# Performance work log

Measured on AMD Instinct MI355X. Metric: run time of the kernel, lower is better.

The kernel has to match this reference:

```python
import jax, jax.numpy as jnp
import numpy as np

N_HEAD = 8
D_MODEL = 128  # per-head dim == d_model in this 'interpretable' MHA
B, S = 2, 2048
LN_EPS = 1e-3  # keras LayerNormalization default epsilon


def setup_inputs() -> dict:
    key = jax.random.key(0)
    ks = jax.random.split(key, 8)
    sc = 1.0 / np.sqrt(D_MODEL)
    q = jax.random.normal(ks[0], (B, S, D_MODEL), jnp.float32)
    k = jax.random.normal(ks[1], (B, S, D_MODEL), jnp.float32)
    v = jax.random.normal(ks[2], (B, S, D_MODEL), jnp.float32)
    # multiplicative causal mask (lower-triangular ones), broadcast over B,H
    mask = jnp.tril(jnp.ones((S, S), jnp.float32))[None, None, :, :]
    Wq = jax.random.normal(ks[3], (D_MODEL, N_HEAD * D_MODEL), jnp.float32) * sc
    Wk = jax.random.normal(ks[4], (D_MODEL, N_HEAD * D_MODEL), jnp.float32) * sc
    Wv = jax.random.normal(ks[5], (D_MODEL, N_HEAD * D_MODEL), jnp.float32) * sc
    Wo = jax.random.normal(ks[6], (N_HEAD * D_MODEL, D_MODEL), jnp.float32) * sc
    gamma = jnp.ones((D_MODEL,), jnp.float32)
    beta = jnp.zeros((D_MODEL,), jnp.float32)
    return {"q": q, "k": k, "v": v, "mask": mask, "Wq": Wq, "Wk": Wk,
            "Wv": Wv, "Wo": Wo, "gamma": gamma, "beta": beta}


def reference(q, k, v, mask, Wq, Wk, Wv, Wo, gamma, beta):
    b = q.shape[0]
    # projections -> [B, H, S, D]
    def split_heads(x):
        return x.reshape(b, -1, N_HEAD, D_MODEL).transpose(0, 2, 1, 3)
    qs = split_heads(q @ Wq)
    ks_ = split_heads(k @ Wk)
    vs = split_heads(v @ Wv)
    scores = jnp.einsum('bhqd,bhkd->bhqk', qs, ks_) / jnp.sqrt(jnp.float32(D_MODEL))
    scores = scores * mask  # multiplicative mask (NOT additive -inf)
    attn = jax.nn.softmax(scores, axis=-1)
    # dropout layers are identity at inference
    out = jnp.einsum('bhqk,bhkd->bhqd', attn, vs)
    out = out.transpose(0, 2, 1, 3).reshape(b, -1, N_HEAD * D_MODEL)
    out = out @ Wo
    # keras LayerNorm (axis=-1, eps=1e-3)
    mu = jnp.mean(out, axis=-1, keepdims=True)
    var = jnp.var(out, axis=-1, keepdims=True)
    out = (out - mu) * jax.lax.rsqrt(var + LN_EPS) * gamma + beta
    return out
```

## Files before the change

### kernel.cpp

```cpp
#include <hip/hip_runtime.h>
#include <math.h>

#define B 2
#define S 2048
#define H 8
#define D 128
#define DM 1024
#define BH 16

typedef unsigned short u16;
typedef __attribute__((ext_vector_type(8))) short bf16x8;
typedef __attribute__((ext_vector_type(8))) unsigned short u16x8;
typedef __attribute__((ext_vector_type(4))) float f32x4;

__device__ __forceinline__ float bf2f(u16 x) {
    union { unsigned u; float f; } c; c.u = ((unsigned)x) << 16; return c.f;
}
__device__ __forceinline__ u16 f2bf(float f) {
    union { unsigned u; float f; } c; c.f = f;
    unsigned u = c.u; u += 0x7fffu + ((u >> 16) & 1u);
    return (u16)(u >> 16);
}
__device__ __forceinline__ u16 ftr(float f) {
    union { unsigned u; float f; } c; c.f = f;
    return (u16)(c.u >> 16);
}

#define MFMA16(a, b, c) __builtin_amdgcn_mfma_f32_16x16x32_bf16((a), (b), (c), 0, 0, 0)

__global__ __launch_bounds__(256) void prep_kernel(
    const float* __restrict__ Wq, const float* __restrict__ Wk, const float* __restrict__ Wv,
    const float* __restrict__ Wo, u16* __restrict__ WT, u16* __restrict__ WoT)
{
    __shared__ __align__(16) u16 Wl[128][132];
    int tid = threadIdx.x, by = blockIdx.x;
    if (by < 16) {
        int k0 = by * 64;
#pragma unroll
        for (int i = 0; i < 8; i++) {
            int e = i * 256 + tid; int kk = e >> 5, n4 = e & 31;
            float4 w4 = *(const float4*)&Wo[(size_t)(k0 + kk) * D + n4 * 4];
            ushort4 p; p.x = ftr(w4.x); p.y = ftr(w4.y); p.z = ftr(w4.z); p.w = ftr(w4.w);
            *(ushort4*)&Wl[kk][n4 * 4] = p;
        }
        __syncthreads();
#pragma unroll
        for (int i = 0; i < 4; i++) {
            int e = i * 256 + tid; int n = e >> 3, ko = e & 7;
            u16x8 g;
#pragma unroll
            for (int j = 0; j < 8; j++) g[j] = Wl[ko * 8 + j][n];
            *(u16x8*)&WoT[(size_t)n * DM + k0 + ko * 8] = g;
        }
    } else {
        int tile = by - 16;
        int t = tile >> 3, h = tile & 7;
        const float* W = (t == 0) ? Wq : (t == 1) ? Wk : Wv;
        int col0 = h * 128;
#pragma unroll
        for (int i = 0; i < 16; i++) {
            int e = i * 256 + tid; int kk = e >> 5, n4 = e & 31;
            float4 w4 = *(const float4*)&W[(size_t)kk * DM + col0 + n4 * 4];
            ushort4 p; p.x = ftr(w4.x); p.y = ftr(w4.y); p.z = ftr(w4.z); p.w = ftr(w4.w);
            *(ushort4*)&Wl[kk][n4 * 4] = p;
        }
        __syncthreads();
        u16* WTt = WT + (size_t)tile * (128 * 128);
#pragma unroll
        for (int i = 0; i < 8; i++) {
            int e = i * 256 + tid; int n = e >> 4, ko = e & 15;
            u16x8 g;
#pragma unroll
            for (int j = 0; j < 8; j++) g[j] = Wl[ko * 8 + j][n];
            *(u16x8*)&WTt[(size_t)n * 128 + ko * 8] = g;
        }
    }
}

__global__ __launch_bounds__(256) void proj_kernel(
    const float* __restrict__ q, const float* __restrict__ k, const float* __restrict__ v,
    const u16* __restrict__ WT,
    u16* __restrict__ Qo, u16* __restrict__ Ko, u16* __restrict__ VTo,
    float* __restrict__ Csum)
{
    __shared__ __align__(16) u16 Xs[64][136];
    __shared__ __align__(16) u16 Ws[128][136];
    int tid = threadIdx.x;
    int m0 = blockIdx.x * 64;
    int by = blockIdx.y;
    int t = by >> 3;
    int h = by & 7;
    const float* X = (t == 0) ? q : (t == 1) ? k : v;
    const u16* WTt = WT + (size_t)(t * 8 + h) * (128 * 128);

#pragma unroll
    for (int i = 0; i < 8; i++) {
        int e = i * 256 + tid; int r = e >> 5, c4 = e & 31;
        float4 x4 = *(const float4*)&X[(size_t)(m0 + r) * D + c4 * 4];
        ushort4 p; p.x = ftr(x4.x); p.y = ftr(x4.y); p.z = ftr(x4.z); p.w = ftr(x4.w);
        *(ushort4*)&Xs[r][c4 * 4] = p;
    }
#pragma unroll
    for (int i = 0; i < 8; i++) {
        int e = i * 256 + tid; int n = e >> 4, c8 = e & 15;
        *(u16x8*)&Ws[n][c8 * 8] = *(const u16x8*)&WTt[(size_t)n * 128 + c8 * 8];
    }
    __syncthreads();

    int w = tid >> 6, lane = tid & 63, quad = lane >> 4, ln = lane & 15;
    bf16x8 aX[4];
#pragma unroll
    for (int ks = 0; ks < 4; ks++)
        aX[ks] = *(const bf16x8*)&Xs[w * 16 + ln][ks * 32 + quad * 8];

    f32x4 zero = {0.f, 0.f, 0.f, 0.f};
    f32x4 acc[8];
#pragma unroll
    for (int nt = 0; nt < 8; nt++) acc[nt] = zero;

#pragma unroll
    for (int ks = 0; ks < 4; ks++) {
        bf16x8 bW[8];
#pragma unroll
        for (int nt = 0; nt < 8; nt++)
            bW[nt] = *(const bf16x8*)&Ws[nt * 16 + ln][ks * 32 + quad * 8];
#pragma unroll
        for (int nt = 0; nt < 8; nt++)
            acc[nt] = MFMA16(aX[ks], bW[nt], acc[nt]);
    }

    int bb = m0 >> 11, ss0 = m0 & 2047;
    int bh = bb * 8 + h;
    __syncthreads();
    if (t < 2) {
        u16 (*Ct)[136] = Xs;
        u16* O = (t == 0) ? Qo : Ko;
#pragma unroll
        for (int nt = 0; nt < 8; nt++)
#pragma unroll
            for (int r = 0; r < 4; r++)
                Ct[w * 16 + quad * 4 + r][nt * 16 + ln] = f2bf(acc[nt][r]);
        __syncthreads();
#pragma unroll
        for (int i = 0; i < 4; i++) {
            int e = i * 256 + tid; int r = e >> 4, c8 = e & 15;
            *(u16x8*)&O[((size_t)bh * S + ss0 + r) * D + c8 * 8] = *(const u16x8*)&Ct[r][c8 * 8];
        }
    } else {
        u16 (*Ct)[68] = (u16 (*)[68])&Xs[0][0];
#pragma unroll
        for (int nt = 0; nt < 8; nt++)
#pragma unroll
            for (int r = 0; r < 4; r++)
                Ct[nt * 16 + ln][w * 16 + quad * 4 + r] = f2bf(acc[nt][r]);
        __syncthreads();
#pragma unroll
        for (int i = 0; i < 4; i++) {
            int e = i * 256 + tid; int dloc = e >> 3, c8 = e & 7;
            *(u16x8*)&VTo[((size_t)bh * D + dloc) * S + ss0 + c8 * 8] =
                *(const u16x8*)&Ct[dloc][c8 * 8];
        }
        if (tid < 128) {
            int d = tid;
            float s = 0.f;
#pragma unroll
            for (int i = 0; i < 8; i++) {
                u16x8 v8 = *(const u16x8*)&Ct[d][i * 8];
#pragma unroll
                for (int j = 0; j < 8; j++) s += bf2f(v8[j]);
            }
            Csum[((size_t)bh * 32 + (ss0 >> 6)) * D + d] = s;
        }
    }
}

__global__ __launch_bounds__(512, 2) void attn_kernel(
    const u16* __restrict__ Qb, const u16* __restrict__ Kb, const u16* __restrict__ VTg,
    const float* __restrict__ Csum, u16* __restrict__ HOb)
{
    __shared__ __align__(16) u16 Qs[2][64][136];
    __shared__ __align__(16) u16 Ks[128][136];
    __shared__ __align__(16) u16 Vt[128][136];
    __shared__ __align__(16) u16 Ps[2][64][136];
    __shared__ float Lred[2][4][64];

    int tid = threadIdx.x;
    int bh = blockIdx.x;
    int bx = blockIdx.y;
    int nhi = (31 - bx) / 2 + 1, nlo = bx / 2 + 1;
    int w = tid >> 6, qt = w >> 2, wq = w & 3, lane = tid & 63, quad = lane >> 4, ln = lane & 15;
    int qb = qt ? bx : (31 - bx);
    int q0 = qb * 64;
    int nq = qt ? nlo : nhi;
    const u16* Qp  = Qb  + (size_t)bh * S * D;
    const u16* Kp  = Kb  + (size_t)bh * S * D;
    const u16* VTp = VTg + (size_t)bh * D * S;

#pragma unroll
    for (int i = 0; i < 4; i++) {
        int e = i * 512 + tid; int r2 = e >> 4, c8 = e & 15;
        int qtt = r2 >> 6, r = r2 & 63;
        int q0s = (qtt ? bx : (31 - bx)) * 64;
        *(u16x8*)&Qs[qtt][r][c8 * 8] = *(const u16x8*)&Qp[(size_t)(q0s + r) * D + c8 * 8];
    }
    __syncthreads();
    bf16x8 aQ[4][4];
#pragma unroll
    for (int rf = 0; rf < 4; rf++)
#pragma unroll
        for (int ks = 0; ks < 4; ks++)
            aQ[rf][ks] = *(const bf16x8*)&Qs[qt][rf * 16 + ln][ks * 32 + quad * 8];

    f32x4 zero = {0.f, 0.f, 0.f, 0.f};
    f32x4 accPV[4][2], acc_l[4];
#pragma unroll
    for (int rf = 0; rf < 4; rf++) { accPV[rf][0] = zero; accPV[rf][1] = zero; acc_l[rf] = zero; }
    bf16x8 bOnes;
#pragma unroll
    for (int j = 0; j < 8; j++) bOnes[j] = (short)0x3F80;
    const float scale = 0.08838834764831845f;

    for (int kt = 0; kt < nhi; kt++) {
        __syncthreads();
        int k0 = kt * 128;
#pragma unroll
        for (int i = 0; i < 4; i++) {
            int e = i * 512 + tid; int r = e >> 4, c8 = e & 15;
            *(u16x8*)&Ks[r][c8 * 8] = *(const u16x8*)&Kp[(size_t)(k0 + r) * D + c8 * 8];
        }
#pragma unroll
        for (int i = 0; i < 4; i++) {
            int e = i * 512 + tid; int dd = e >> 4, c8 = e & 15;
            *(u16x8*)&Vt[dd][c8 * 8] = *(const u16x8*)&VTp[(size_t)dd * S + k0 + c8 * 8];
        }
        __syncthreads();
        bool active = (qt == 0) || (kt < nlo);
        if (active) {
            f32x4 s[4][2];
#pragma unroll
            for (int rf = 0; rf < 4; rf++) { s[rf][0] = zero; s[rf][1] = zero; }
#pragma unroll
            for (int ks = 0; ks < 4; ks++) {
                bf16x8 b0 = *(const bf16x8*)&Ks[wq * 32 + ln][ks * 32 + quad * 8];
                bf16x8 b1 = *(const bf16x8*)&Ks[wq * 32 + 16 + ln][ks * 32 + quad * 8];
#pragma unroll
                for (int rf = 0; rf < 4; rf++) {
                    s[rf][0] = MFMA16(aQ[rf][ks], b0, s[rf][0]);
                    s[rf][1] = MFMA16(aQ[rf][ks], b1, s[rf][1]);
                }
            }
#pragma unroll
            for (int rf = 0; rf < 4; rf++)
#pragma unroll
                for (int ct = 0; ct < 2; ct++) {
                    int col = k0 + wq * 32 + ct * 16 + ln;
                    int rowb = q0 + rf * 16 + quad * 4;
#pragma unroll
                    for (int r = 0; r < 4; r++) {
                        float tv = (col <= rowb + r) ? s[rf][ct][r] : 0.f;
                        float p = __expf(tv * scale);
                        Ps[qt][rf * 16 + quad * 4 + r][wq * 32 + ct * 16 + ln] = f2bf(p);
                    }
                }
        }
        __syncthreads();
        if (active) {
#pragma unroll
            for (int ks = 0; ks < 4; ks++) {
                bf16x8 aP[4];
#pragma unroll
                for (int rf = 0; rf < 4; rf++)
                    aP[rf] = *(const bf16x8*)&Ps[qt][rf * 16 + ln][ks * 32 + quad * 8];
                bf16x8 v0 = *(const bf16x8*)&Vt[wq * 32 + ln][ks * 32 + quad * 8];
                bf16x8 v1 = *(const bf16x8*)&Vt[wq * 32 + 16 + ln][ks * 32 + quad * 8];
                if (ks == wq) {
#pragma unroll
                    for (int rf = 0; rf < 4; rf++) acc_l[rf] = MFMA16(aP[rf], bOnes, acc_l[rf]);
                }
#pragma unroll
                for (int rf = 0; rf < 4; rf++) {
                    accPV[rf][0] = MFMA16(aP[rf], v0, accPV[rf][0]);
                    accPV[rf][1] = MFMA16(aP[rf], v1, accPV[rf][1]);
                }
            }
        }
    }

    __syncthreads();
    if (ln == 0) {
#pragma unroll
        for (int rf = 0; rf < 4; rf++)
#pragma unroll
            for (int r = 0; r < 4; r++)
                Lred[qt][wq][rf * 16 + quad * 4 + r] = acc_l[rf][r];
    }
    __syncthreads();

    int nt64 = 2 * nq;
    float suf0 = 0.f, suf1 = 0.f;
    for (int c = 31; c >= nt64; c--) {
        const float* cp = &Csum[((size_t)(bh * 32 + c)) * D + wq * 32];
        suf0 += cp[ln];
        suf1 += cp[16 + ln];
    }
    int scount = S - nq * 128;
    int b = bh >> 3, h = bh & 7;
#pragma unroll
    for (int rf = 0; rf < 4; rf++)
#pragma unroll
        for (int r = 0; r < 4; r++) {
            int row = rf * 16 + quad * 4 + r;
            int srow = q0 + row;
            float l = Lred[qt][0][row] + Lred[qt][1][row] + Lred[qt][2][row] + Lred[qt][3][row]
                      + (float)scount;
            float inv = 1.f / l;
            size_t base = ((size_t)(b * S + srow)) * DM + h * D + wq * 32;
            HOb[base + ln]      = f2bf((accPV[rf][0][r] + suf0) * inv);
            HOb[base + 16 + ln] = f2bf((accPV[rf][1][r] + suf1) * inv);
        }
}

__global__ __launch_bounds__(256) void out_ln_kernel(
    const u16* __restrict__ HOb, const u16* __restrict__ WoT,
    const float* __restrict__ gamma, const float* __restrict__ beta,
    float* __restrict__ out)
{
    __shared__ __align__(16) u16 HOs[16][1048];
    __shared__ float Cs[16][132];
    int tid = threadIdx.x;
    int m0 = blockIdx.x * 16;
    int w = tid >> 6, lane = tid & 63, quad = lane >> 4, ln = lane & 15;
#pragma unroll
    for (int i = 0; i < 8; i++) {
        int e = i * 256 + tid; int r = e >> 7, c8 = e & 127;
        *(u16x8*)&HOs[r][c8 * 8] = *(const u16x8*)&HOb[(size_t)(m0 + r) * DM + c8 * 8];
    }
    __syncthreads();
    f32x4 zero = {0.f, 0.f, 0.f, 0.f};
    f32x4 acc[2] = {zero, zero};
#pragma unroll 4
    for (int ks = 0; ks < 32; ks++) {
        bf16x8 aH = *(const bf16x8*)&HOs[ln][ks * 32 + quad * 8];
        bf16x8 w0 = *(const bf16x8*)&WoT[(size_t)(w * 32 + ln) * DM + ks * 32 + quad * 8];
        bf16x8 w1 = *(const bf16x8*)&WoT[(size_t)(w * 32 + 16 + ln) * DM + ks * 32 + quad * 8];
        acc[0] = MFMA16(aH, w0, acc[0]);
        acc[1] = MFMA16(aH, w1, acc[1]);
    }
#pragma unroll
    for (int ct = 0; ct < 2; ct++)
#pragma unroll
        for (int r = 0; r < 4; r++)
            Cs[quad * 4 + r][w * 32 + ct * 16 + ln] = acc[ct][r];
    __syncthreads();

    int row = tid >> 4, t16 = tid & 15;
    float xv[8], sum = 0.f, sq = 0.f;
#pragma unroll
    for (int j = 0; j < 8; j++) {
        float x = Cs[row][t16 * 8 + j];
        xv[j] = x; sum += x; sq += x * x;
    }
#pragma unroll
    for (int off = 1; off < 16; off <<= 1) {
        sum += __shfl_xor(sum, off);
        sq  += __shfl_xor(sq, off);
    }
    float mu = sum * (1.f / 128.f);
    float var = sq * (1.f / 128.f) - mu * mu;
    float rstd = rsqrtf(var + 1e-3f);
    float o[8];
#pragma unroll
    for (int j = 0; j < 8; j++) {
        int c = t16 * 8 + j;
        o[j] = (xv[j] - mu) * rstd * gamma[c] + beta[c];
    }
    float* op = &out[(size_t)(m0 + row) * D + t16 * 8];
    *(float4*)&op[0] = *(float4*)&o[0];
    *(float4*)&op[4] = *(float4*)&o[4];
}

extern "C" void kernel_launch(void* const* d_in, const int* in_sizes, int n_in,
                              void* d_out, int out_size, void* d_ws, size_t ws_size,
                              hipStream_t stream)
{
    const float* q     = (const float*)d_in[0];
    const float* k     = (const float*)d_in[1];
    const float* v     = (const float*)d_in[2];
    const float* Wq    = (const float*)d_in[4];
    const float* Wk    = (const float*)d_in[5];
    const float* Wv    = (const float*)d_in[6];
    const float* Wo    = (const float*)d_in[7];
    const float* gamma = (const float*)d_in[8];
    const float* beta  = (const float*)d_in[9];

    u16* ws16 = (u16*)d_ws;
    u16* Qb  = ws16;
    u16* Kb  = ws16 + 4194304;
    u16* VT  = ws16 + 8388608;
    u16* HOb = ws16 + 12582912;
    u16* WoT = ws16 + 16777216;
    u16* WT  = ws16 + 16908288;
    float* Csum = (float*)((char*)d_ws + 35651584);

    prep_kernel<<<40, 256, 0, stream>>>(Wq, Wk, Wv, Wo, WT, WoT);
    proj_kernel<<<dim3(64, 24), 256, 0, stream>>>(q, k, v, WT, Qb, Kb, VT, Csum);
    attn_kernel<<<dim3(BH, 16), 512, 0, stream>>>(Qb, Kb, VT, Csum, HOb);
    out_ln_kernel<<<256, 256, 0, stream>>>(HOb, WoT, gamma, beta, (float*)d_out);
}
```

Before: 155.6 us.

## Prefetch next K/V tile into registers during attention compute; add MFMA priority hints

Moves the first K/Vt tile load into the prologue. Each loop iteration now issues global loads for the next K and V^T tile into registers before the QK^T and PV MFMA work, then writes them to shared memory after the compute. This hides global-memory latency behind matrix math. It also raises wave priority around the MFMA blocks, at the cost of 8 extra u16x8 registers per thread and one extra barrier per iteration.

```diff
diff --git a/kernel.cpp b/kernel.cpp
--- a/kernel.cpp
+++ b/kernel.cpp
@@ -203,6 +203,16 @@
         int q0s = (qtt ? bx : (31 - bx)) * 64;
         *(u16x8*)&Qs[qtt][r][c8 * 8] = *(const u16x8*)&Qp[(size_t)(q0s + r) * D + c8 * 8];
     }
+#pragma unroll
+    for (int i = 0; i < 4; i++) {
+        int e = i * 512 + tid; int r = e >> 4, c8 = e & 15;
+        *(u16x8*)&Ks[r][c8 * 8] = *(const u16x8*)&Kp[(size_t)r * D + c8 * 8];
+    }
+#pragma unroll
+    for (int i = 0; i < 4; i++) {
+        int e = i * 512 + tid; int dd = e >> 4, c8 = e & 15;
+        *(u16x8*)&Vt[dd][c8 * 8] = *(const u16x8*)&VTp[(size_t)dd * S + c8 * 8];
+    }
     __syncthreads();
     bf16x8 aQ[4][4];
 #pragma unroll
@@ -220,25 +230,29 @@
     for (int j = 0; j < 8; j++) bOnes[j] = (short)0x3F80;
     const float scale = 0.08838834764831845f;
 
+    u16x8 kreg[4], vreg[4];
     for (int kt = 0; kt < nhi; kt++) {
-        __syncthreads();
         int k0 = kt * 128;
-#pragma unroll
-        for (int i = 0; i < 4; i++) {
-            int e = i * 512 + tid; int r = e >> 4, c8 = e & 15;
-            *(u16x8*)&Ks[r][c8 * 8] = *(const u16x8*)&Kp[(size_t)(k0 + r) * D + c8 * 8];
-        }
-#pragma unroll
-        for (int i = 0; i < 4; i++) {
-            int e = i * 512 + tid; int dd = e >> 4, c8 = e & 15;
-            *(u16x8*)&Vt[dd][c8 * 8] = *(const u16x8*)&VTp[(size_t)dd * S + k0 + c8 * 8];
-        }
-        __syncthreads();
+        int k1 = k0 + 128;
+        bool pf = (kt + 1 < nhi);
+        if (pf) {
+#pragma unroll
+            for (int i = 0; i < 4; i++) {
+                int e = i * 512 + tid; int r = e >> 4, c8 = e & 15;
+                kreg[i] = *(const u16x8*)&Kp[(size_t)(k1 + r) * D + c8 * 8];
+            }
+#pragma unroll
+            for (int i = 0; i < 4; i++) {
+                int e = i * 512 + tid; int dd = e >> 4, c8 = e & 15;
+                vreg[i] = *(const u16x8*)&VTp[(size_t)dd * S + k1 + c8 * 8];
+            }
+        }
         bool active = (qt == 0) || (kt < nlo);
         if (active) {
             f32x4 s[4][2];
 #pragma unroll
             for (int rf = 0; rf < 4; rf++) { s[rf][0] = zero; s[rf][1] = zero; }
+            __builtin_amdgcn_s_setprio(1);
 #pragma unroll
             for (int ks = 0; ks < 4; ks++) {
                 bf16x8 b0 = *(const bf16x8*)&Ks[wq * 32 + ln][ks * 32 + quad * 8];
@@ -249,6 +263,7 @@
                     s[rf][1] = MFMA16(aQ[rf][ks], b1, s[rf][1]);
                 }
             }
+            __builtin_amdgcn_s_setprio(0);
 #pragma unroll
             for (int rf = 0; rf < 4; rf++)
 #pragma unroll
@@ -265,6 +280,7 @@
         }
         __syncthreads();
         if (active) {
+            __builtin_amdgcn_s_setprio(1);
 #pragma unroll
             for (int ks = 0; ks < 4; ks++) {
                 bf16x8 aP[4];
@@ -283,7 +299,22 @@
                     accPV[rf][1] = MFMA16(aP[rf], v1, accPV[rf][1]);
                 }
             }
-        }
+            __builtin_amdgcn_s_setprio(0);
+        }
+        __syncthreads();
+        if (pf) {
+#pragma unroll
+            for (int i = 0; i < 4; i++) {
+                int e = i * 512 + tid; int r = e >> 4, c8 = e & 15;
+                *(u16x8*)&Ks[r][c8 * 8] = kreg[i];
+            }
+#pragma unroll
+            for (int i = 0; i < 4; i++) {
+                int e = i * 512 + tid; int dd = e >> 4, c8 = e & 15;
+                *(u16x8*)&Vt[dd][c8 * 8] = vreg[i];
+            }
+        }
+        __syncthreads();
     }
 
     __syncthreads();
```

New measurement: 154.4 us. Within noise of the previous version (-0.8%).

## Restructure attention into single-Q-tile blocks with register-prefetched K/V tiles

Applied to the files above, without the earlier changes.

The attention kernel now uses 256-thread blocks, each handling one 64-row query tile, instead of 512-thread blocks that paired a heavy and a light tile. Each warp keeps its K fragment in registers, and the next tile's K and V^T are prefetched into registers while the current tile computes. The key tile shrinks from 128 to 64, the causal mask runs only on the diagonal tile, and MFMA sections are bracketed with s_setprio. This aims to cut shared-memory traffic and sync stalls and to overlap global loads with compute, at the cost of more blocks with uneven work and more registers per thread.

```diff
diff --git a/kernel.cpp b/kernel.cpp
--- a/kernel.cpp
+++ b/kernel.cpp
@@ -174,42 +174,41 @@
     }
 }
 
-__global__ __launch_bounds__(512, 2) void attn_kernel(
+__global__ __launch_bounds__(256, 3) void attn_kernel(
     const u16* __restrict__ Qb, const u16* __restrict__ Kb, const u16* __restrict__ VTg,
     const float* __restrict__ Csum, u16* __restrict__ HOb)
 {
-    __shared__ __align__(16) u16 Qs[2][64][136];
-    __shared__ __align__(16) u16 Ks[128][136];
-    __shared__ __align__(16) u16 Vt[128][136];
-    __shared__ __align__(16) u16 Ps[2][64][136];
-    __shared__ float Lred[2][4][64];
+    __shared__ __align__(16) u16 Qs[64][136];
+    __shared__ __align__(16) u16 Ps[64][72];
+    __shared__ __align__(16) u16 Vt[128][72];
+    __shared__ float Lred[4][64];
 
     int tid = threadIdx.x;
     int bh = blockIdx.x;
-    int bx = blockIdx.y;
-    int nhi = (31 - bx) / 2 + 1, nlo = bx / 2 + 1;
-    int w = tid >> 6, qt = w >> 2, wq = w & 3, lane = tid & 63, quad = lane >> 4, ln = lane & 15;
-    int qb = qt ? bx : (31 - bx);
+    int y  = blockIdx.y;
+    int qb = (y < 16) ? (31 - y) : (y - 16);
     int q0 = qb * 64;
-    int nq = qt ? nlo : nhi;
+    int ntile = qb + 1;
+    int w = tid >> 6, lane = tid & 63, quad = lane >> 4, ln = lane & 15;
     const u16* Qp  = Qb  + (size_t)bh * S * D;
     const u16* Kp  = Kb  + (size_t)bh * S * D;
     const u16* VTp = VTg + (size_t)bh * D * S;
 
 #pragma unroll
     for (int i = 0; i < 4; i++) {
-        int e = i * 512 + tid; int r2 = e >> 4, c8 = e & 15;
-        int qtt = r2 >> 6, r = r2 & 63;
-        int q0s = (qtt ? bx : (31 - bx)) * 64;
-        *(u16x8*)&Qs[qtt][r][c8 * 8] = *(const u16x8*)&Qp[(size_t)(q0s + r) * D + c8 * 8];
-    }
-    __syncthreads();
-    bf16x8 aQ[4][4];
-#pragma unroll
-    for (int rf = 0; rf < 4; rf++)
-#pragma unroll
-        for (int ks = 0; ks < 4; ks++)
-            aQ[rf][ks] = *(const bf16x8*)&Qs[qt][rf * 16 + ln][ks * 32 + quad * 8];
+        int e = i * 256 + tid; int r = e >> 4, c8 = e & 15;
+        *(u16x8*)&Qs[r][c8 * 8] = *(const u16x8*)&Qp[(size_t)(q0 + r) * D + c8 * 8];
+    }
+#pragma unroll
+    for (int i = 0; i < 4; i++) {
+        int e = i * 256 + tid; int dd = e >> 3, c8 = e & 7;
+        *(u16x8*)&Vt[dd][c8 * 8] = *(const u16x8*)&VTp[(size_t)dd * S + c8 * 8];
+    }
+    bf16x8 kfrag[4];
+#pragma unroll
+    for (int ks = 0; ks < 4; ks++)
+        kfrag[ks] = *(const bf16x8*)&Kp[(size_t)(w * 16 + ln) * D + ks * 32 + quad * 8];
+    __syncthreads();
 
     f32x4 zero = {0.f, 0.f, 0.f, 0.f};
     f32x4 accPV[4][2], acc_l[4];
@@ -220,90 +219,101 @@
     for (int j = 0; j < 8; j++) bOnes[j] = (short)0x3F80;
     const float scale = 0.08838834764831845f;
 
-    for (int kt = 0; kt < nhi; kt++) {
-        __syncthreads();
-        int k0 = kt * 128;
-#pragma unroll
-        for (int i = 0; i < 4; i++) {
-            int e = i * 512 + tid; int r = e >> 4, c8 = e & 15;
-            *(u16x8*)&Ks[r][c8 * 8] = *(const u16x8*)&Kp[(size_t)(k0 + r) * D + c8 * 8];
-        }
-#pragma unroll
-        for (int i = 0; i < 4; i++) {
-            int e = i * 512 + tid; int dd = e >> 4, c8 = e & 15;
-            *(u16x8*)&Vt[dd][c8 * 8] = *(const u16x8*)&VTp[(size_t)dd * S + k0 + c8 * 8];
-        }
-        __syncthreads();
-        bool active = (qt == 0) || (kt < nlo);
-        if (active) {
-            f32x4 s[4][2];
-#pragma unroll
-            for (int rf = 0; rf < 4; rf++) { s[rf][0] = zero; s[rf][1] = zero; }
-#pragma unroll
-            for (int ks = 0; ks < 4; ks++) {
-                bf16x8 b0 = *(const bf16x8*)&Ks[wq * 32 + ln][ks * 32 + quad * 8];
-                bf16x8 b1 = *(const bf16x8*)&Ks[wq * 32 + 16 + ln][ks * 32 + quad * 8];
-#pragma unroll
-                for (int rf = 0; rf < 4; rf++) {
-                    s[rf][0] = MFMA16(aQ[rf][ks], b0, s[rf][0]);
-                    s[rf][1] = MFMA16(aQ[rf][ks], b1, s[rf][1]);
+    bf16x8 kn[4];
+    u16x8 vreg[4];
+    for (int kt = 0; kt < ntile; kt++) {
+        int k1 = (kt + 1) * 64;
+        bool pf = (kt + 1 < ntile);
+        if (pf) {
+#pragma unroll
+            for (int ks = 0; ks < 4; ks++)
+                kn[ks] = *(const bf16x8*)&Kp[(size_t)(k1 + w * 16 + ln) * D + ks * 32 + quad * 8];
+#pragma unroll
+            for (int i = 0; i < 4; i++) {
+                int e = i * 256 + tid; int dd = e >> 3, c8 = e & 7;
+                vreg[i] = *(const u16x8*)&VTp[(size_t)dd * S + k1 + c8 * 8];
+            }
+        }
+        f32x4 s[4];
+#pragma unroll
+        for (int rf = 0; rf < 4; rf++) s[rf] = zero;
+        __builtin_amdgcn_s_setprio(1);
+#pragma unroll
+        for (int ks = 0; ks < 4; ks++) {
+#pragma unroll
+            for (int rf = 0; rf < 4; rf++) {
+                bf16x8 aQ = *(const bf16x8*)&Qs[rf * 16 + ln][ks * 32 + quad * 8];
+                s[rf] = MFMA16(aQ, kfrag[ks], s[rf]);
+            }
+        }
+        __builtin_amdgcn_s_setprio(0);
+        int colb = kt * 64 + w * 16 + ln;
+        if (kt == qb) {
+#pragma unroll
+            for (int rf = 0; rf < 4; rf++) {
+                int rowb = q0 + rf * 16 + quad * 4;
+#pragma unroll
+                for (int r = 0; r < 4; r++) {
+                    float tv = (colb <= rowb + r) ? s[rf][r] : 0.f;
+                    Ps[rf * 16 + quad * 4 + r][w * 16 + ln] = f2bf(__expf(tv * scale));
                 }
             }
+        } else {
 #pragma unroll
             for (int rf = 0; rf < 4; rf++)
 #pragma unroll
-                for (int ct = 0; ct < 2; ct++) {
-                    int col = k0 + wq * 32 + ct * 16 + ln;
-                    int rowb = q0 + rf * 16 + quad * 4;
-#pragma unroll
-                    for (int r = 0; r < 4; r++) {
-                        float tv = (col <= rowb + r) ? s[rf][ct][r] : 0.f;
-                        float p = __expf(tv * scale);
-                        Ps[qt][rf * 16 + quad * 4 + r][wq * 32 + ct * 16 + ln] = f2bf(p);
-                    }
-                }
-        }
-        __syncthreads();
-        if (active) {
-#pragma unroll
-            for (int ks = 0; ks < 4; ks++) {
-                bf16x8 aP[4];
-#pragma unroll
-                for (int rf = 0; rf < 4; rf++)
-                    aP[rf] = *(const bf16x8*)&Ps[qt][rf * 16 + ln][ks * 32 + quad * 8];
-                bf16x8 v0 = *(const bf16x8*)&Vt[wq * 32 + ln][ks * 32 + quad * 8];
-                bf16x8 v1 = *(const bf16x8*)&Vt[wq * 32 + 16 + ln][ks * 32 + quad * 8];
-                if (ks == wq) {
-#pragma unroll
-                    for (int rf = 0; rf < 4; rf++) acc_l[rf] = MFMA16(aP[rf], bOnes, acc_l[rf]);
-                }
-#pragma unroll
-                for (int rf = 0; rf < 4; rf++) {
-                    accPV[rf][0] = MFMA16(aP[rf], v0, accPV[rf][0]);
-                    accPV[rf][1] = MFMA16(aP[rf], v1, accPV[rf][1]);
-                }
-            }
-        }
-    }
-
-    __syncthreads();
+                for (int r = 0; r < 4; r++)
+                    Ps[rf * 16 + quad * 4 + r][w * 16 + ln] = f2bf(__expf(s[rf][r] * scale));
+        }
+        __syncthreads();
+        __builtin_amdgcn_s_setprio(1);
+#pragma unroll
+        for (int ks = 0; ks < 2; ks++) {
+            bf16x8 aP[4];
+#pragma unroll
+            for (int rf = 0; rf < 4; rf++)
+                aP[rf] = *(const bf16x8*)&Ps[rf * 16 + ln][ks * 32 + quad * 8];
+            bf16x8 v0 = *(const bf16x8*)&Vt[w * 32 + ln][ks * 32 + quad * 8];
+            bf16x8 v1 = *(const bf16x8*)&Vt[w * 32 + 16 + ln][ks * 32 + quad * 8];
+            if (((kt * 2 + ks) & 3) == w) {
+#pragma unroll
+                for (int rf = 0; rf < 4; rf++) acc_l[rf] = MFMA16(aP[rf], bOnes, acc_l[rf]);
+            }
+#pragma unroll
+            for (int rf = 0; rf < 4; rf++) {
+                accPV[rf][0] = MFMA16(aP[rf], v0, accPV[rf][0]);
+                accPV[rf][1] = MFMA16(aP[rf], v1, accPV[rf][1]);
+            }
+        }
+        __builtin_amdgcn_s_setprio(0);
+        __syncthreads();
+        if (pf) {
+#pragma unroll
+            for (int i = 0; i < 4; i++) {
+                int e = i * 256 + tid; int dd = e >> 3, c8 = e & 7;
+                *(u16x8*)&Vt[dd][c8 * 8] = vreg[i];
+            }
+#pragma unroll
+            for (int ks = 0; ks < 4; ks++) kfrag[ks] = kn[ks];
+        }
+    }
+
     if (ln == 0) {
 #pragma unroll
         for (int rf = 0; rf < 4; rf++)
 #pragma unroll
             for (int r = 0; r < 4; r++)
-                Lred[qt][wq][rf * 16 + quad * 4 + r] = acc_l[rf][r];
-    }
-    __syncthreads();
-
-    int nt64 = 2 * nq;
+                Lred[w][rf * 16 + quad * 4 + r] = acc_l[rf][r];
+    }
+    __syncthreads();
+
     float suf0 = 0.f, suf1 = 0.f;
-    for (int c = 31; c >= nt64; c--) {
-        const float* cp = &Csum[((size_t)(bh * 32 + c)) * D + wq * 32];
+    for (int c = 31; c >= ntile; c--) {
+        const float* cp = &Csum[((size_t)(bh * 32 + c)) * D + w * 32];
         suf0 += cp[ln];
         suf1 += cp[16 + ln];
     }
-    int scount = S - nq * 128;
+    int scount = S - ntile * 64;
     int b = bh >> 3, h = bh & 7;
 #pragma unroll
     for (int rf = 0; rf < 4; rf++)
@@ -311,10 +321,10 @@
         for (int r = 0; r < 4; r++) {
             int row = rf * 16 + quad * 4 + r;
             int srow = q0 + row;
-            float l = Lred[qt][0][row] + Lred[qt][1][row] + Lred[qt][2][row] + Lred[qt][3][row]
+            float l = Lred[0][row] + Lred[1][row] + Lred[2][row] + Lred[3][row]
                       + (float)scount;
             float inv = 1.f / l;
-            size_t base = ((size_t)(b * S + srow)) * DM + h * D + wq * 32;
+            size_t base = ((size_t)(b * S + srow)) * DM + h * D + w * 32;
             HOb[base + ln]      = f2bf((accPV[rf][0][r] + suf0) * inv);
             HOb[base + 16 + ln] = f2bf((accPV[rf][1][r] + suf1) * inv);
         }
@@ -404,6 +414,6 @@
 
     prep_kernel<<<40, 256, 0, stream>>>(Wq, Wk, Wv, Wo, WT, WoT);
     proj_kernel<<<dim3(64, 24), 256, 0, stream>>>(q, k, v, WT, Qb, Kb, VT, Csum);
-    attn_kernel<<<dim3(BH, 16), 512, 0, stream>>>(Qb, Kb, VT, Csum, HOb);
+    attn_kernel<<<dim3(BH, 32), 256, 0, stream>>>(Qb, Kb, VT, Csum, HOb);
     out_ln_kernel<<<256, 256, 0, stream>>>(HOb, WoT, gamma, beta, (float*)d_out);
 }
```

After: 166.2 us. 1.07x slower.

## Prefetch K/V tiles with async global-to-LDS loads, double-buffered and XOR-swizzled

Applied to the files above, without the earlier changes.

Replaces the register-staged global-to-LDS copies in the attention loop with direct async global_load_lds transfers. The next K tile is prefetched into a second buffer during QK^T, and the next V tile is loaded right after the PV stage, so memory traffic overlaps compute. LDS rows drop their padding in favour of an XOR swizzle to avoid bank conflicts, and s_setprio is raised around the MFMA blocks. The Q staging buffer now reuses the Vt space. This depends on the barrier waiting for the async LDS writes, and the extra K buffer raises LDS use.

```diff
diff --git a/kernel.cpp b/kernel.cpp
--- a/kernel.cpp
+++ b/kernel.cpp
@@ -27,6 +27,14 @@
 }
 
 #define MFMA16(a, b, c) __builtin_amdgcn_mfma_f32_16x16x32_bf16((a), (b), (c), 0, 0, 0)
+
+__device__ __forceinline__ void gload_lds16(const void* g, void* l) {
+    __builtin_amdgcn_global_load_lds(
+        (__attribute__((address_space(1))) void*)(unsigned long long)(g),
+        (__attribute__((address_space(3))) void*)(unsigned long long)(l), 16, 0, 0);
+}
+
+#define SWZ(R, CC) ((((CC) ^ ((R) & 7)) * 8))
 
 __global__ __launch_bounds__(256) void prep_kernel(
     const float* __restrict__ Wq, const float* __restrict__ Wk, const float* __restrict__ Wv,
@@ -178,10 +186,9 @@
     const u16* __restrict__ Qb, const u16* __restrict__ Kb, const u16* __restrict__ VTg,
     const float* __restrict__ Csum, u16* __restrict__ HOb)
 {
-    __shared__ __align__(16) u16 Qs[2][64][136];
-    __shared__ __align__(16) u16 Ks[128][136];
-    __shared__ __align__(16) u16 Vt[128][136];
-    __shared__ __align__(16) u16 Ps[2][64][136];
+    __shared__ __align__(16) u16 Ks[2][128][128];
+    __shared__ __align__(16) u16 Vt[128][128];
+    __shared__ __align__(16) u16 Ps[2][64][132];
     __shared__ float Lred[2][4][64];
 
     int tid = threadIdx.x;
@@ -198,18 +205,31 @@
 
 #pragma unroll
     for (int i = 0; i < 4; i++) {
-        int e = i * 512 + tid; int r2 = e >> 4, c8 = e & 15;
-        int qtt = r2 >> 6, r = r2 & 63;
+        int ci = i * 512 + tid;
+        int r = ci >> 4, c = ci & 15;
+        int sc = c ^ (r & 7);
+        int qtt = r >> 6, rr = r & 63;
         int q0s = (qtt ? bx : (31 - bx)) * 64;
-        *(u16x8*)&Qs[qtt][r][c8 * 8] = *(const u16x8*)&Qp[(size_t)(q0s + r) * D + c8 * 8];
+        gload_lds16(&Qp[(size_t)(q0s + rr) * D + sc * 8], (u16*)&Vt[0][0] + ci * 8);
+        gload_lds16(&Kp[(size_t)r * D + sc * 8], (u16*)&Ks[0][0][0] + ci * 8);
     }
     __syncthreads();
     bf16x8 aQ[4][4];
 #pragma unroll
     for (int rf = 0; rf < 4; rf++)
 #pragma unroll
-        for (int ks = 0; ks < 4; ks++)
-            aQ[rf][ks] = *(const bf16x8*)&Qs[qt][rf * 16 + ln][ks * 32 + quad * 8];
+        for (int ks = 0; ks < 4; ks++) {
+            int R = qt * 64 + rf * 16 + ln;
+            aQ[rf][ks] = *(const bf16x8*)&Vt[R][SWZ(R, ks * 4 + quad)];
+        }
+    __syncthreads();
+#pragma unroll
+    for (int i = 0; i < 4; i++) {
+        int ci = i * 512 + tid;
+        int dd = ci >> 4, c = ci & 15;
+        int sc = c ^ (dd & 7);
+        gload_lds16(&VTp[(size_t)dd * S + sc * 8], (u16*)&Vt[0][0] + ci * 8);
+    }
 
     f32x4 zero = {0.f, 0.f, 0.f, 0.f};
     f32x4 accPV[4][2], acc_l[4];
@@ -221,34 +241,37 @@
     const float scale = 0.08838834764831845f;
 
     for (int kt = 0; kt < nhi; kt++) {
-        __syncthreads();
+        int cur = kt & 1, nxt = cur ^ 1;
         int k0 = kt * 128;
-#pragma unroll
-        for (int i = 0; i < 4; i++) {
-            int e = i * 512 + tid; int r = e >> 4, c8 = e & 15;
-            *(u16x8*)&Ks[r][c8 * 8] = *(const u16x8*)&Kp[(size_t)(k0 + r) * D + c8 * 8];
-        }
-#pragma unroll
-        for (int i = 0; i < 4; i++) {
-            int e = i * 512 + tid; int dd = e >> 4, c8 = e & 15;
-            *(u16x8*)&Vt[dd][c8 * 8] = *(const u16x8*)&VTp[(size_t)dd * S + k0 + c8 * 8];
-        }
-        __syncthreads();
+        bool pf = (kt + 1 < nhi);
+        if (pf) {
+#pragma unroll
+            for (int i = 0; i < 4; i++) {
+                int ci = i * 512 + tid;
+                int r = ci >> 4, c = ci & 15;
+                int sc = c ^ (r & 7);
+                gload_lds16(&Kp[(size_t)(k0 + 128 + r) * D + sc * 8],
+                            (u16*)&Ks[nxt][0][0] + ci * 8);
+            }
+        }
         bool active = (qt == 0) || (kt < nlo);
         if (active) {
             f32x4 s[4][2];
 #pragma unroll
             for (int rf = 0; rf < 4; rf++) { s[rf][0] = zero; s[rf][1] = zero; }
+            __builtin_amdgcn_s_setprio(1);
 #pragma unroll
             for (int ks = 0; ks < 4; ks++) {
-                bf16x8 b0 = *(const bf16x8*)&Ks[wq * 32 + ln][ks * 32 + quad * 8];
-                bf16x8 b1 = *(const bf16x8*)&Ks[wq * 32 + 16 + ln][ks * 32 + quad * 8];
+                int rb0 = wq * 32 + ln, rb1 = wq * 32 + 16 + ln;
+                bf16x8 b0 = *(const bf16x8*)&Ks[cur][rb0][SWZ(rb0, ks * 4 + quad)];
+                bf16x8 b1 = *(const bf16x8*)&Ks[cur][rb1][SWZ(rb1, ks * 4 + quad)];
 #pragma unroll
                 for (int rf = 0; rf < 4; rf++) {
                     s[rf][0] = MFMA16(aQ[rf][ks], b0, s[rf][0]);
                     s[rf][1] = MFMA16(aQ[rf][ks], b1, s[rf][1]);
                 }
             }
+            __builtin_amdgcn_s_setprio(0);
 #pragma unroll
             for (int rf = 0; rf < 4; rf++)
 #pragma unroll
@@ -265,14 +288,16 @@
         }
         __syncthreads();
         if (active) {
+            __builtin_amdgcn_s_setprio(1);
 #pragma unroll
             for (int ks = 0; ks < 4; ks++) {
                 bf16x8 aP[4];
 #pragma unroll
                 for (int rf = 0; rf < 4; rf++)
                     aP[rf] = *(const bf16x8*)&Ps[qt][rf * 16 + ln][ks * 32 + quad * 8];
-                bf16x8 v0 = *(const bf16x8*)&Vt[wq * 32 + ln][ks * 32 + quad * 8];
-                bf16x8 v1 = *(const bf16x8*)&Vt[wq * 32 + 16 + ln][ks * 32 + quad * 8];
+                int rv0 = wq * 32 + ln, rv1 = wq * 32 + 16 + ln;
+                bf16x8 v0 = *(const bf16x8*)&Vt[rv0][SWZ(rv0, ks * 4 + quad)];
+                bf16x8 v1 = *(const bf16x8*)&Vt[rv1][SWZ(rv1, ks * 4 + quad)];
                 if (ks == wq) {
 #pragma unroll
                     for (int rf = 0; rf < 4; rf++) acc_l[rf] = MFMA16(aP[rf], bOnes, acc_l[rf]);
@@ -282,6 +307,18 @@
                     accPV[rf][0] = MFMA16(aP[rf], v0, accPV[rf][0]);
                     accPV[rf][1] = MFMA16(aP[rf], v1, accPV[rf][1]);
                 }
+            }
+            __builtin_amdgcn_s_setprio(0);
+        }
+        __syncthreads();
+        if (pf) {
+#pragma unroll
+            for (int i = 0; i < 4; i++) {
+                int ci = i * 512 + tid;
+                int dd = ci >> 4, c = ci & 15;
+                int sc = c ^ (dd & 7);
+                gload_lds16(&VTp[(size_t)dd * S + k0 + 128 + sc * 8],
+                            (u16*)&Vt[0][0] + ci * 8);
             }
         }
     }
```

Measured after the change: 148.5 us. 1.05x faster.
